# Kernel tuning notes

Hardware: AMD Instinct MI355X
Metric: run time of the kernel (lower is better)

The kernel has to match this reference:

```python
import jax, jax.numpy as jnp
import numpy as np
from jax import lax

HEADS = 8
DIM_HEAD = 64
INNER = HEADS * DIM_HEAD  # 512
DIM = 256
TOP_K = 512  # top_k=-1 -> Lk // heads = 4096 // 8
LN_EPS = 1e-5


def chan_ln(x, g, b):
    # LayerNorm over channel dim (axis=1) of [b,c,D,H,W]
    mu = jnp.mean(x, axis=1, keepdims=True)
    var = jnp.mean((x - mu) ** 2, axis=1, keepdims=True)
    xn = (x - mu) * lax.rsqrt(var + LN_EPS)
    return xn * g[None, :, None, None, None] + b[None, :, None, None, None]


def l1_cdist(K, Q):
    # K: [B,N,D], Q: [B,M,D] -> [B,N,M]; scan over feature dim to avoid a [B,N,M,D] intermediate
    Kt = jnp.moveaxis(K, -1, 0)  # [D,B,N]
    Qt = jnp.moveaxis(Q, -1, 0)  # [D,B,M]
    acc0 = jnp.zeros((K.shape[0], K.shape[1], Q.shape[1]), K.dtype)
    def step(acc, kq):
        kd, qd = kq
        return acc + jnp.abs(kd[:, :, None] - qd[:, None, :]), None
    acc, _ = lax.scan(step, acc0, (Kt, Qt))
    return acc


def l2norm_ax(t, axis):
    n = jnp.sqrt(jnp.sum(t * t, axis=axis, keepdims=True))
    return t / jnp.maximum(n, 1e-12)


def setup_inputs() -> dict:
    key = jax.random.key(0)
    ks = jax.random.split(key, 12)
    b, Dq, Hq, Wq = 2, 16, 32, 32
    Dc, Hc, Wc = 16, 16, 16
    Lk = Dc * Hc * Wc  # 4096
    return {
        "query_source": jax.random.normal(ks[0], (b, DIM, Dq, Hq, Wq), jnp.float32),
        "context": jax.random.normal(ks[1], (b, DIM, Dc, Hc, Wc), jnp.float32),
        "rand_idx": jax.random.randint(ks[2], (b * HEADS, TOP_K), 0, 4096),
        "g_ctx": jnp.ones((DIM,), jnp.float32),
        "b_ctx": jnp.zeros((DIM,), jnp.float32),
        "g_qs": jnp.ones((DIM,), jnp.float32),
        "b_qs": jnp.zeros((DIM,), jnp.float32),
        "w_kv": jax.random.normal(ks[3], (2 * INNER, DIM), jnp.float32) * 0.02,
        "w_q": jax.random.normal(ks[4], (INNER, DIM), jnp.float32) * 0.02,
        "w_out": jax.random.normal(ks[5], (DIM, INNER), jnp.float32) * 0.02,
        "g_out": jnp.ones((DIM,), jnp.float32),
        "b_out": jnp.zeros((DIM,), jnp.float32),
        "gamma": jnp.full((1,), 0.5, jnp.float32),
    }


def reference(query_source, context, rand_idx, g_ctx, b_ctx, g_qs, b_qs,
              w_kv, w_q, w_out, g_out, b_out, gamma):
    b, c, Dq, Hq, Wq = query_source.shape
    Lq = Dq * Hq * Wq
    Lk = context.shape[2] * context.shape[3] * context.shape[4]

    ctx = chan_ln(context, g_ctx, b_ctx)
    qsn = chan_ln(query_source, g_qs, b_qs)

    # 1x1x1 convs == channel matmuls
    kv = jnp.einsum('oc,bcdhw->bodhw', w_kv, ctx)
    k, v = jnp.split(kv, 2, axis=1)
    q = jnp.einsum('oc,bcdhw->bodhw', w_q, qsn)

    def fold(t):  # [b, inner, ...] -> [b, heads, dim_head, L]
        return t.reshape(t.shape[0], HEADS, DIM_HEAD, -1)
    q, k, v = fold(q), fold(k), fold(v)
    # l2norm over dim_head channels (torch dim=1 after (b h) fold)
    q = l2norm_ax(q, 2)
    k = l2norm_ax(k, 2)
    # -> [b, heads, L, dim_head]
    q = jnp.swapaxes(q, 2, 3)
    k = jnp.swapaxes(k, 2, 3)
    v = jnp.swapaxes(v, 2, 3)

    BH = b * HEADS
    qf = q.reshape(BH, Lq, DIM_HEAD)
    kf = k.reshape(BH, Lk, DIM_HEAD)
    vf = v.reshape(BH, Lk, DIM_HEAD)

    # random-query-anchored token pruning
    Q_small = jnp.take_along_axis(qf, rand_idx[:, :, None], axis=1)  # [BH, TOP_K, dh]
    dist = l1_cdist(kf, Q_small)                                     # [BH, Lk, TOP_K]
    min_d = jnp.min(dist, axis=2)                                    # [BH, Lk]
    _, idx = lax.top_k(-min_d, TOP_K)                                # smallest distances
    ks_sel = jnp.take_along_axis(kf, idx[:, :, None], axis=1)        # [BH, TOP_K, dh]
    vs_sel = jnp.take_along_axis(vf, idx[:, :, None], axis=1)

    ks4 = ks_sel.reshape(b, HEADS, TOP_K, DIM_HEAD)
    vs4 = vs_sel.reshape(b, HEADS, TOP_K, DIM_HEAD)

    # SDPA with scale=1.0, no dropout (eval)
    scores = jnp.einsum('bhqd,bhkd->bhqk', q, ks4)
    attn = jax.nn.softmax(scores, axis=-1)
    out = jnp.einsum('bhqk,bhkd->bhqd', attn, vs4)  # [b,H,Lq,dh]

    out = out.reshape(b, HEADS, Dq, Hq, Wq, DIM_HEAD)
    out = jnp.transpose(out, (0, 1, 5, 2, 3, 4)).reshape(b, INNER, Dq, Hq, Wq)
    out = jnp.einsum('oc,bcdhw->bodhw', w_out, out)
    out = chan_ln(out, g_out, b_out)
    return gamma[0] * out + query_source
```

## Files before the change

### kernel.cpp

```cpp
#include <hip/hip_runtime.h>
#include <hip/hip_bf16.h>
#include <math.h>

#define DIMC  256
#define HEADS 8
#define DH    64
#define INNER 512
#define TOPK  512
#define LQ    16384
#define LKE   4096
#define NB    2
#define NBH   16

typedef __attribute__((ext_vector_type(8))) short bf16x8;
typedef __attribute__((ext_vector_type(4))) float f32x4;
typedef __attribute__((ext_vector_type(16))) unsigned u32x16;

__device__ __forceinline__ unsigned short f2bf(float f) {
    unsigned u = __float_as_uint(f);
    u += 0x7FFFu + ((u >> 16) & 1u);
    return (unsigned short)(u >> 16);
}
__device__ __forceinline__ float bf2f(unsigned short b) {
    return __uint_as_float(((unsigned)b) << 16);
}
__device__ __forceinline__ f32x4 mfma16(bf16x8 a, bf16x8 b, f32x4 c) {
    return __builtin_amdgcn_mfma_f32_16x16x32_bf16(a, b, c, 0, 0, 0);
}
__device__ __forceinline__ unsigned f2q16(float v) {
    return (unsigned)((int)rintf(v * 32000.0f) + 32768) & 0xFFFFu;
}

__global__ void stats_all_kernel(const float* __restrict__ ctx, const float* __restrict__ qs,
                                 float* __restrict__ mu_c, float* __restrict__ rs_c,
                                 float* __restrict__ mu_q, float* __restrict__ rs_q) {
    int idx = blockIdx.x * 256 + threadIdx.x;
    const float* x; float* mu; float* rs; int L; int li;
    if (idx < NB * LKE) { x = ctx; mu = mu_c; rs = rs_c; L = LKE; li = idx; }
    else { li = idx - NB * LKE; if (li >= NB * LQ) return; x = qs; mu = mu_q; rs = rs_q; L = LQ; }
    int b = li / L, l = li - b * L;
    const float* p = x + (size_t)b * DIMC * L + l;
    float s = 0.f, sq = 0.f;
    for (int c = 0; c < DIMC; c++) {
        float v = p[(size_t)c * L];
        s += v; sq += v * v;
    }
    float m = s * (1.0f / DIMC);
    float var = fmaxf(sq * (1.0f / DIMC) - m * m, 0.f);
    mu[li] = m;
    rs[li] = rsqrtf(var + 1e-5f);
}

template<bool WRITELO>
__global__ __launch_bounds__(256) void ln_transpose_kernel(
    const float* __restrict__ x, const float* __restrict__ mu, const float* __restrict__ rs,
    const float* __restrict__ g, const float* __restrict__ beta, int L,
    unsigned short* __restrict__ xhi, unsigned short* __restrict__ xlo) {
    int lt = blockIdx.x, ct = blockIdx.y, b = blockIdx.z;
    int l0 = lt * 64, c0 = ct * 64;
    int t = threadIdx.x;
    __shared__ float T[64][65];
#pragma unroll
    for (int r = 0; r < 16; r++) {
        int f = r * 256 + t;
        int l = f & 63, c = f >> 6;
        int loc = b * L + l0 + l;
        float v = x[((size_t)b * DIMC + c0 + c) * L + l0 + l];
        T[c][l] = (v - mu[loc]) * rs[loc] * g[c0 + c] + beta[c0 + c];
    }
    __syncthreads();
#pragma unroll
    for (int r = 0; r < 16; r++) {
        int f = r * 256 + t;
        int c = f & 63, l = f >> 6;
        float v = T[c][l];
        unsigned short hi = f2bf(v);
        size_t di = ((size_t)b * L + l0 + l) * DIMC + c0 + c;
        xhi[di] = hi;
        if (WRITELO) xlo[di] = f2bf(v - bf2f(hi));
    }
}

template<int MODE>
__global__ __launch_bounds__(256) void gemm_mfma_kernel(
    const float* __restrict__ wmat,
    const unsigned short* __restrict__ xhi, const unsigned short* __restrict__ xlo,
    void* __restrict__ dst0, void* __restrict__ dst1, void* __restrict__ dst2) {
    constexpr int K = (MODE == 2) ? 512 : 256;
    constexpr int N = (MODE == 0) ? LKE : LQ;
    constexpr bool MAYSPLIT = (MODE == 0);
    int n0 = blockIdx.x * 128;
    int by = blockIdx.y;
    int bb = blockIdx.z;
    int t = threadIdx.x, w = t >> 6, lane = t & 63;
    int wm = w >> 1, wn = w & 1;
    int lanelo = lane & 15, lanehi = lane >> 4;

    __shared__ __align__(16) char Wh[16384];
    __shared__ __align__(16) char Xh[16384];
    __shared__ __align__(16) char Wl[MAYSPLIT ? 16384 : 16];
    __shared__ __align__(16) char Xl[MAYSPLIT ? 16384 : 16];

    bool split = MAYSPLIT && (by < 4);

    const float* wsrc = wmat + (size_t)by * 128 * K;
    const unsigned short* xsh = xhi + ((size_t)bb * N + n0) * K;
    const unsigned short* xsl = xlo + ((size_t)bb * N + n0) * K;

    f32x4 acc[4][4];
#pragma unroll
    for (int mi = 0; mi < 4; mi++)
#pragma unroll
        for (int ni = 0; ni < 4; ni++) acc[mi][ni] = (f32x4){0.f, 0.f, 0.f, 0.f};

    for (int k0 = 0; k0 < K; k0 += 64) {
        if (k0) __syncthreads();
#pragma unroll
        for (int gg = 0; gg < 4; gg++) {
            int e = gg * 2048 + t * 8;
            int row = e >> 6, kc = e & 63;
            const float* wp = wsrc + (size_t)row * K + k0 + kc;
            bf16x8 hi, lo;
#pragma unroll
            for (int i = 0; i < 8; i++) {
                float v = wp[i];
                unsigned short h = f2bf(v);
                hi[i] = (short)h;
                if (MAYSPLIT) lo[i] = (short)f2bf(v - bf2f(h));
            }
            int off = (row * 128 + kc * 2) ^ ((row & 7) << 4);
            *(bf16x8*)(Wh + off) = hi;
            *(bf16x8*)(Xh + off) = *(const bf16x8*)(xsh + (size_t)row * K + k0 + kc);
            if (split) {
                *(bf16x8*)(Wl + off) = lo;
                *(bf16x8*)(Xl + off) = *(const bf16x8*)(xsl + (size_t)row * K + k0 + kc);
            }
        }
        __syncthreads();
#pragma unroll
        for (int kk = 0; kk < 2; kk++) {
            bf16x8 ah[4], bh_[4];
#pragma unroll
            for (int mi = 0; mi < 4; mi++) {
                int row = wm * 64 + mi * 16 + lanelo;
                int off = (row * 128 + kk * 64 + lanehi * 16) ^ ((row & 7) << 4);
                ah[mi] = *(const bf16x8*)(Wh + off);
            }
#pragma unroll
            for (int ni = 0; ni < 4; ni++) {
                int row = wn * 64 + ni * 16 + lanelo;
                int off = (row * 128 + kk * 64 + lanehi * 16) ^ ((row & 7) << 4);
                bh_[ni] = *(const bf16x8*)(Xh + off);
            }
#pragma unroll
            for (int mi = 0; mi < 4; mi++)
#pragma unroll
                for (int ni = 0; ni < 4; ni++)
                    acc[mi][ni] = mfma16(ah[mi], bh_[ni], acc[mi][ni]);
            if (split) {
                bf16x8 al[4], bl_[4];
#pragma unroll
                for (int mi = 0; mi < 4; mi++) {
                    int row = wm * 64 + mi * 16 + lanelo;
                    int off = (row * 128 + kk * 64 + lanehi * 16) ^ ((row & 7) << 4);
                    al[mi] = *(const bf16x8*)(Wl + off);
                }
#pragma unroll
                for (int ni = 0; ni < 4; ni++) {
                    int row = wn * 64 + ni * 16 + lanelo;
                    int off = (row * 128 + kk * 64 + lanehi * 16) ^ ((row & 7) << 4);
                    bl_[ni] = *(const bf16x8*)(Xl + off);
                }
#pragma unroll
                for (int mi = 0; mi < 4; mi++)
#pragma unroll
                    for (int ni = 0; ni < 4; ni++) {
                        acc[mi][ni] = mfma16(ah[mi], bl_[ni], acc[mi][ni]);
                        acc[mi][ni] = mfma16(al[mi], bh_[ni], acc[mi][ni]);
                    }
            }
        }
    }

    bool donorm = (MODE == 1) || (MODE == 0 && by < 4);
    float inv[4];
    if (donorm) {
#pragma unroll
        for (int ni = 0; ni < 4; ni++) {
            float s = 0.f;
#pragma unroll
            for (int mi = 0; mi < 4; mi++)
#pragma unroll
                for (int rg = 0; rg < 4; rg++) s += acc[mi][ni][rg] * acc[mi][ni][rg];
            s += __shfl_xor(s, 16);
            s += __shfl_xor(s, 32);
            inv[ni] = 1.0f / fmaxf(sqrtf(s), 1e-12f);
        }
    }
#pragma unroll
    for (int mi = 0; mi < 4; mi++) {
        int rowg = by * 128 + wm * 64 + mi * 16 + lanehi * 4;
#pragma unroll
        for (int ni = 0; ni < 4; ni++) {
            int l = n0 + wn * 64 + ni * 16 + lanelo;
            if (MODE == 0) {
                bool isk = rowg < 512;
                float sc = isk ? inv[ni] : 1.0f;
                int h = (rowg >> 6) & 7, d0 = rowg & 63;
                float4 v = make_float4(acc[mi][ni][0] * sc, acc[mi][ni][1] * sc,
                                       acc[mi][ni][2] * sc, acc[mi][ni][3] * sc);
                float* dp = isk ? (float*)dst0 : (float*)dst1;
                size_t base = ((size_t)(bb * HEADS + h) * LKE + l) * 64 + d0;
                *(float4*)&dp[base] = v;
                if (isk) {
                    uint2 pk;
                    pk.x = f2q16(v.x) | (f2q16(v.y) << 16);
                    pk.y = f2q16(v.z) | (f2q16(v.w) << 16);
                    *(uint2*)&((unsigned*)dst2)[(((size_t)(bb * HEADS + h) * LKE + l) * 64 + d0) / 2] = pk;
                }
            } else if (MODE == 1) {
                int h = rowg >> 6, d0 = rowg & 63;
                ushort4 u;
                u.x = f2bf(acc[mi][ni][0] * inv[ni]);
                u.y = f2bf(acc[mi][ni][1] * inv[ni]);
                u.z = f2bf(acc[mi][ni][2] * inv[ni]);
                u.w = f2bf(acc[mi][ni][3] * inv[ni]);
                unsigned short* qp = (unsigned short*)dst0;
                *(ushort4*)&qp[((size_t)(bb * HEADS + h) * LQ + l) * 64 + d0] = u;
            } else {
                float4 v = make_float4(acc[mi][ni][0], acc[mi][ni][1],
                                       acc[mi][ni][2], acc[mi][ni][3]);
                float* pp = (float*)dst0;
                *(float4*)&pp[((size_t)bb * LQ + l) * 256 + rowg] = v;
            }
        }
    }
}

__global__ __launch_bounds__(256) void qsample_kernel(
    const float* __restrict__ x, const float* __restrict__ mu, const float* __restrict__ rs,
    const float* __restrict__ g, const float* __restrict__ beta,
    const float* __restrict__ w, const int* __restrict__ ridx,
    unsigned* __restrict__ Qint) {
    int lt = blockIdx.x, bh = blockIdx.y;
    int b = bh >> 3, h = bh & 7;
    int t = threadIdx.x, tx = t & 15, ty = t >> 4;
    __shared__ float Ws[64][33];
    __shared__ float Xs[32][65];
    __shared__ float Cs[64][65];
    __shared__ float nf[64];
    __shared__ int lidx[64];
    if (t < 64) lidx[t] = ridx[bh * TOPK + lt * 64 + t];
    __syncthreads();
    float acc[4][4];
#pragma unroll
    for (int a = 0; a < 4; a++)
#pragma unroll
        for (int c2 = 0; c2 < 4; c2++) acc[a][c2] = 0.f;
    for (int kc = 0; kc < DIMC; kc += 32) {
#pragma unroll
        for (int r = 0; r < 8; r++) {
            int f = r * 256 + t;
            int oi = f >> 5, kj = f & 31;
            Ws[oi][kj] = w[(size_t)(h * 64 + oi) * DIMC + kc + kj];
        }
#pragma unroll
        for (int r = 0; r < 8; r++) {
            int f = r * 256 + t;
            int kj = f >> 6, lj = f & 63;
            int l = lidx[lj];
            int loc = b * LQ + l;
            float v = x[(size_t)b * DIMC * LQ + (size_t)(kc + kj) * LQ + l];
            Xs[kj][lj] = (v - mu[loc]) * rs[loc] * g[kc + kj] + beta[kc + kj];
        }
        __syncthreads();
#pragma unroll
        for (int kj = 0; kj < 32; kj++) {
            float wr[4], xr[4];
#pragma unroll
            for (int a = 0; a < 4; a++) wr[a] = Ws[ty * 4 + a][kj];
#pragma unroll
            for (int c2 = 0; c2 < 4; c2++) xr[c2] = Xs[kj][tx * 4 + c2];
#pragma unroll
            for (int a = 0; a < 4; a++)
#pragma unroll
                for (int c2 = 0; c2 < 4; c2++) acc[a][c2] += wr[a] * xr[c2];
        }
        __syncthreads();
    }
#pragma unroll
    for (int a = 0; a < 4; a++)
#pragma unroll
        for (int c2 = 0; c2 < 4; c2++) Cs[ty * 4 + a][tx * 4 + c2] = acc[a][c2];
    __syncthreads();
    if (t < 64) {
        float sq = 0.f;
        for (int o = 0; o < 64; o++) { float v = Cs[o][t]; sq += v * v; }
        nf[t] = 1.0f / fmaxf(sqrtf(sq), 1e-12f);
    }
    __syncthreads();
#pragma unroll
    for (int r = 0; r < 8; r++) {
        int f = r * 256 + t;
        int dp = f & 31, lj = f >> 5;
        float v0 = Cs[dp * 2][lj] * nf[lj];
        float v1 = Cs[dp * 2 + 1][lj] * nf[lj];
        Qint[((size_t)bh * TOPK + (size_t)lt * 64 + lj) * 32 + dp] =
            f2q16(v0) | (f2q16(v1) << 16);
    }
}

__global__ __launch_bounds__(256) __attribute__((amdgpu_waves_per_eu(4, 4)))
void cdist_sad_kernel(
    const unsigned* __restrict__ kint,
    const unsigned* __restrict__ Qint,
    unsigned* __restrict__ min_d4) {
    int bh = blockIdx.y;
    int key = blockIdx.x * 256 + threadIdx.x;
    int qz = blockIdx.z;
    const unsigned* kp = kint + ((size_t)bh * LKE + key) * 32;
    unsigned k[32];
#pragma unroll
    for (int d8 = 0; d8 < 8; d8++) {
        uint4 v = *(const uint4*)(kp + d8 * 4);
        k[d8 * 4 + 0] = v.x; k[d8 * 4 + 1] = v.y;
        k[d8 * 4 + 2] = v.z; k[d8 * 4 + 3] = v.w;
    }
#pragma unroll
    for (int d = 0; d < 32; d++) asm volatile("" : "+v"(k[d]));

    unsigned long long qaddr = (unsigned long long)(const void*)
        (Qint + ((size_t)bh * TOPK + (size_t)qz * (TOPK / 4)) * 32);
    u32x16 qa0, qa1, qb0, qb1;
    asm volatile(
        "s_load_dwordx16 %0, %2, 0x00\n\t"
        "s_load_dwordx16 %1, %2, 0x40"
        : "=s"(qa0), "=s"(qa1) : "s"(qaddr));
    unsigned best = 0xFFFFFFFFu;

#define S1(ACC, KK, QQ) asm("v_sad_u16 %0, %1, %2, %0" : "+v"(ACC) : "v"(KK), "s"(QQ));
#define S16(QV, KB) \
    S1(a0, k[KB + 0], QV[0])  S1(a1, k[KB + 1], QV[1]) \
    S1(a2, k[KB + 2], QV[2])  S1(a3, k[KB + 3], QV[3]) \
    S1(a0, k[KB + 4], QV[4])  S1(a1, k[KB + 5], QV[5]) \
    S1(a2, k[KB + 6], QV[6])  S1(a3, k[KB + 7], QV[7]) \
    S1(a0, k[KB + 8], QV[8])  S1(a1, k[KB + 9], QV[9]) \
    S1(a2, k[KB + 10], QV[10]) S1(a3, k[KB + 11], QV[11]) \
    S1(a0, k[KB + 12], QV[12]) S1(a1, k[KB + 13], QV[13]) \
    S1(a2, k[KB + 14], QV[14]) S1(a3, k[KB + 15], QV[15])

    for (int qi = 0; qi < TOPK / 4; qi += 2) {
        asm volatile(
            "s_load_dwordx16 %0, %2, 0x80\n\t"
            "s_load_dwordx16 %1, %2, 0xc0"
            : "=s"(qb0), "=s"(qb1) : "s"(qaddr));
        asm volatile("s_waitcnt lgkmcnt(2)" : "+s"(qa0), "+s"(qa1));
        {
            unsigned a0 = 0, a1 = 0, a2 = 0, a3 = 0;
            S16(qa0, 0) S16(qa1, 16)
            best = min(best, (a0 + a1) + (a2 + a3));
        }
        qaddr += 256;
        asm volatile(
            "s_load_dwordx16 %0, %2, 0x00\n\t"
            "s_load_dwordx16 %1, %2, 0x40"
            : "=s"(qa0), "=s"(qa1) : "s"(qaddr));
        asm volatile("s_waitcnt lgkmcnt(2)" : "+s"(qb0), "+s"(qb1));
        {
            unsigned a0 = 0, a1 = 0, a2 = 0, a3 = 0;
            S16(qb0, 0) S16(qb1, 16)
            best = min(best, (a0 + a1) + (a2 + a3));
        }
    }
#undef S16
#undef S1
    min_d4[((size_t)qz * NBH + bh) * LKE + key] = best;
}

__global__ void select_topk_kernel(const unsigned* __restrict__ min_d4, int* __restrict__ isel) {
    int bh = blockIdx.x;
    int t = threadIdx.x;
    __shared__ unsigned su[LKE];
    __shared__ int hist[256];
    __shared__ int scan[256];
    __shared__ int sb[2];
    for (int i = t; i < LKE; i += 256) {
        unsigned a = min(min_d4[(size_t)bh * LKE + i],
                         min_d4[(size_t)(NBH + bh) * LKE + i]);
        unsigned b = min(min_d4[(size_t)(2 * NBH + bh) * LKE + i],
                         min_d4[(size_t)(3 * NBH + bh) * LKE + i]);
        su[i] = min(a, b);
    }
    unsigned prefix = 0, mask = 0;
    int need = TOPK;
    for (int shift = 24; shift >= 0; shift -= 8) {
        hist[t] = 0;
        __syncthreads();
        for (int i = t; i < LKE; i += 256) {
            unsigned u = su[i];
            if ((u & mask) == prefix) atomicAdd(&hist[(u >> shift) & 255], 1);
        }
        __syncthreads();
        scan[t] = hist[t];
        __syncthreads();
#pragma unroll
        for (int d = 1; d < 256; d <<= 1) {
            int v = (t >= d) ? scan[t - d] : 0;
            __syncthreads();
            scan[t] += v;
            __syncthreads();
        }
        int excl = (t == 0) ? 0 : scan[t - 1];
        if (scan[t] >= need && excl < need) {
            sb[0] = t;
            sb[1] = need - excl;
        }
        __syncthreads();
        prefix |= ((unsigned)sb[0]) << shift;
        mask |= (255u << shift);
        need = sb[1];
        __syncthreads();
    }
    if (t < 64) {
        int pos = 0, eqseen = 0;
        unsigned long long lanem1 = (t == 0) ? 0ull : ((1ull << t) - 1ull);
        for (int i0 = 0; i0 < LKE; i0 += 64) {
            unsigned u = su[i0 + t];
            bool lt = (u < prefix);
            bool eq = (u == prefix);
            unsigned long long be = __ballot(eq);
            int eqbefore = __popcll(be & lanem1);
            bool take = lt || (eq && (eqseen + eqbefore) < need);
            unsigned long long bt = __ballot(take);
            if (take) isel[bh * TOPK + pos + __popcll(bt & lanem1)] = i0 + t;
            pos += __popcll(bt);
            eqseen += __popcll(be);
        }
    }
}

__global__ __launch_bounds__(256) void gather_kv_kernel(
    const float* __restrict__ kf, const float* __restrict__ vf,
    const int* __restrict__ isel,
    unsigned short* __restrict__ kselh, unsigned short* __restrict__ vTh) {
    int bh = blockIdx.y, kc = blockIdx.x * 64;
    int t = threadIdx.x;
    __shared__ float T[64][65];
    __shared__ int rows[64];
    if (t < 64) rows[t] = isel[bh * TOPK + kc + t];
    __syncthreads();
#pragma unroll
    for (int r = 0; r < 16; r++) {
        int f = r * 256 + t;
        int key = f >> 6, d = f & 63;
        kselh[((size_t)bh * TOPK + kc + key) * 64 + d] =
            f2bf(kf[((size_t)bh * LKE + rows[key]) * 64 + d]);
    }
#pragma unroll
    for (int r = 0; r < 4; r++) {
        int c = r * 256 + t;
        int row = c >> 4, c4 = c & 15;
        float4 v = *(const float4*)(vf + ((size_t)bh * LKE + rows[row]) * 64 + c4 * 4);
        T[row][c4 * 4 + 0] = v.x; T[row][c4 * 4 + 1] = v.y;
        T[row][c4 * 4 + 2] = v.z; T[row][c4 * 4 + 3] = v.w;
    }
    __syncthreads();
#pragma unroll
    for (int r = 0; r < 16; r++) {
        int f = r * 256 + t;
        int d = f >> 6, key = f & 63;
        vTh[(size_t)bh * 64 * TOPK + (size_t)d * TOPK + kc + key] = f2bf(T[key][d]);
    }
}

__global__ __launch_bounds__(256) void attn_mfma_kernel(
    const unsigned short* __restrict__ qh,
    const unsigned short* __restrict__ kselh,
    const unsigned short* __restrict__ vTh,
    unsigned short* __restrict__ afT) {
    int bh = blockIdx.y, rt = blockIdx.x;
    int bq = bh >> 3, h = bh & 7;
    int t = threadIdx.x, w = t >> 6, lane = t & 63;
    __shared__ unsigned short Ks[2][64 * 64];
    __shared__ unsigned short Vts[2][64 * 64];
    __shared__ unsigned short Ps[4][2][16 * 64];

    const unsigned short* qb = qh + ((size_t)bh * LQ + (size_t)rt * 128) * 64;
    const unsigned short* kb = kselh + (size_t)bh * TOPK * 64;
    const unsigned short* vb = vTh + (size_t)bh * 64 * TOPK;

    int lanelo = lane & 15, lanehi = lane >> 4;

    int row0s = t >> 3, c80 = t & 7;
    int row1s = 32 + (t >> 3), c81 = t & 7;
    int offs0 = (row0s * 128 + c80 * 16) ^ ((row0s & 7) << 4);
    int offs1 = (row1s * 128 + c81 * 16) ^ ((row1s & 7) << 4);

    bf16x8 qfrag[2][2];
#pragma unroll
    for (int s = 0; s < 2; s++)
#pragma unroll
        for (int kk = 0; kk < 2; kk++) {
            int row = s * 64 + w * 16 + lanelo;
            qfrag[s][kk] = *(const bf16x8*)(qb + (size_t)row * 64 + kk * 32 + lanehi * 8);
        }

    {
        *(bf16x8*)((char*)Ks[0] + offs0) = *(const bf16x8*)(kb + row0s * 64 + c80 * 8);
        *(bf16x8*)((char*)Ks[0] + offs1) = *(const bf16x8*)(kb + row1s * 64 + c81 * 8);
        *(bf16x8*)((char*)Vts[0] + offs0) = *(const bf16x8*)(vb + row0s * TOPK + c80 * 8);
        *(bf16x8*)((char*)Vts[0] + offs1) = *(const bf16x8*)(vb + row1s * TOPK + c81 * 8);
    }
    __syncthreads();

    f32x4 o[2][4];
#pragma unroll
    for (int s = 0; s < 2; s++)
#pragma unroll
        for (int m = 0; m < 4; m++) o[s][m] = (f32x4){0.f, 0.f, 0.f, 0.f};
    float part[2][4] = {{0.f, 0.f, 0.f, 0.f}, {0.f, 0.f, 0.f, 0.f}};
    int cur = 0;

    for (int ch = 0; ch < 8; ch++) {
        bf16x8 knx0, knx1, vnx0, vnx1;
        if (ch < 7) {
            int kc0 = (ch + 1) * 64;
            knx0 = *(const bf16x8*)(kb + (kc0 + row0s) * 64 + c80 * 8);
            knx1 = *(const bf16x8*)(kb + (kc0 + row1s) * 64 + c81 * 8);
            vnx0 = *(const bf16x8*)(vb + row0s * TOPK + kc0 + c80 * 8);
            vnx1 = *(const bf16x8*)(vb + row1s * TOPK + kc0 + c81 * 8);
        }
        bf16x8 kfr[4][2];
#pragma unroll
        for (int n = 0; n < 4; n++)
#pragma unroll
            for (int kk = 0; kk < 2; kk++) {
                int row = n * 16 + lanelo;
                kfr[n][kk] = *(const bf16x8*)((char*)Ks[cur] +
                    ((row * 128 + kk * 64 + lanehi * 16) ^ ((row & 7) << 4)));
            }
#pragma unroll
        for (int s = 0; s < 2; s++) {
            f32x4 sv[4];
#pragma unroll
            for (int n = 0; n < 4; n++) {
                sv[n] = (f32x4){0.f, 0.f, 0.f, 0.f};
#pragma unroll
                for (int kk = 0; kk < 2; kk++)
                    sv[n] = mfma16(qfrag[s][kk], kfr[n][kk], sv[n]);
            }
            unsigned short* pw = Ps[w][s];
#pragma unroll
            for (int n = 0; n < 4; n++) {
#pragma unroll
                for (int rg = 0; rg < 4; rg++) {
                    float p = __expf(sv[n][rg]);
                    unsigned short ph = (unsigned short)(__float_as_uint(p) >> 16);
                    part[s][rg] += bf2f(ph);
                    int row = lanehi * 4 + rg, col = n * 16 + lanelo;
                    *(unsigned short*)((char*)pw +
                        ((row * 128 + col * 2) ^ ((row & 7) << 4))) = ph;
                }
            }
        }
        bf16x8 vfr[4][2];
#pragma unroll
        for (int m = 0; m < 4; m++)
#pragma unroll
            for (int kk = 0; kk < 2; kk++) {
                int row = m * 16 + lanelo;
                vfr[m][kk] = *(const bf16x8*)((char*)Vts[cur] +
                    ((row * 128 + kk * 64 + lanehi * 16) ^ ((row & 7) << 4)));
            }
#pragma unroll
        for (int s = 0; s < 2; s++) {
            bf16x8 pfrag[2];
#pragma unroll
            for (int kk = 0; kk < 2; kk++) {
                int row = lanelo;
                pfrag[kk] = *(const bf16x8*)((char*)Ps[w][s] +
                    ((row * 128 + kk * 64 + lanehi * 16) ^ ((row & 7) << 4)));
            }
#pragma unroll
            for (int m = 0; m < 4; m++)
#pragma unroll
                for (int kk = 0; kk < 2; kk++)
                    o[s][m] = mfma16(pfrag[kk], vfr[m][kk], o[s][m]);
        }
        if (ch < 7) {
            *(bf16x8*)((char*)Ks[cur ^ 1] + offs0) = knx0;
            *(bf16x8*)((char*)Ks[cur ^ 1] + offs1) = knx1;
            *(bf16x8*)((char*)Vts[cur ^ 1] + offs0) = vnx0;
            *(bf16x8*)((char*)Vts[cur ^ 1] + offs1) = vnx1;
        }
        __syncthreads();
        cur ^= 1;
    }
#pragma unroll
    for (int s = 0; s < 2; s++) {
#pragma unroll
        for (int rg = 0; rg < 4; rg++) {
            float v = part[s][rg];
            v += __shfl_xor(v, 1); v += __shfl_xor(v, 2);
            v += __shfl_xor(v, 4); v += __shfl_xor(v, 8);
            float invs = 1.0f / v;
            int l = rt * 128 + s * 64 + w * 16 + lanehi * 4 + rg;
            size_t base = ((size_t)bq * LQ + l) * 512 + h * 64 + lanelo;
#pragma unroll
            for (int m = 0; m < 4; m++)
                afT[base + m * 16] = f2bf(o[s][m][rg] * invs);
        }
    }
}

__global__ void stats_loc_kernel(const float* __restrict__ pre, float* __restrict__ mu,
                                 float* __restrict__ rs) {
    int t = threadIdx.x;
    int grp = t >> 4, ln = t & 15;
    int loc = blockIdx.x * 16 + grp;
    const float4* p = (const float4*)(pre + (size_t)loc * 256);
    float s = 0.f, sq = 0.f;
#pragma unroll
    for (int i = 0; i < 4; i++) {
        float4 v = p[ln + i * 16];
        s += v.x + v.y + v.z + v.w;
        sq += v.x * v.x + v.y * v.y + v.z * v.z + v.w * v.w;
    }
#pragma unroll
    for (int d = 1; d < 16; d <<= 1) {
        s += __shfl_xor(s, d);
        sq += __shfl_xor(sq, d);
    }
    if (ln == 0) {
        float m = s * (1.0f / 256.0f);
        float var = fmaxf(sq * (1.0f / 256.0f) - m * m, 0.f);
        mu[loc] = m;
        rs[loc] = rsqrtf(var + 1e-5f);
    }
}

__global__ __launch_bounds__(256) void final_kernel(
    const float* __restrict__ pre, const float* __restrict__ mu,
    const float* __restrict__ rs, const float* __restrict__ g,
    const float* __restrict__ beta, const float* __restrict__ gamma,
    const float* __restrict__ qs_in, float* __restrict__ out) {
    int lt = blockIdx.x, ot = blockIdx.y, b = blockIdx.z;
    int l0 = lt * 64, o0 = ot * 64;
    int t = threadIdx.x;
    __shared__ float T[64][65];
    float gm = gamma[0];
#pragma unroll
    for (int r = 0; r < 16; r++) {
        int f = r * 256 + t;
        int o = f & 63, l = f >> 6;
        int loc = b * LQ + l0 + l;
        float v = pre[(size_t)loc * 256 + o0 + o];
        T[o][l] = ((v - mu[loc]) * rs[loc] * g[o0 + o] + beta[o0 + o]) * gm;
    }
    __syncthreads();
#pragma unroll
    for (int r = 0; r < 16; r++) {
        int f = r * 256 + t;
        int l = f & 63, o = f >> 6;
        size_t oi = ((size_t)(b * DIMC + o0 + o)) * LQ + l0 + l;
        out[oi] = T[o][l] + qs_in[oi];
    }
}

extern "C" void kernel_launch(void* const* d_in, const int* in_sizes, int n_in,
                              void* d_out, int out_size, void* d_ws, size_t ws_size,
                              hipStream_t stream) {
    const float* qs_in = (const float*)d_in[0];
    const float* ctx   = (const float*)d_in[1];
    const int*   ridx  = (const int*)d_in[2];
    const float* g_ctx = (const float*)d_in[3];
    const float* b_ctx = (const float*)d_in[4];
    const float* g_qs  = (const float*)d_in[5];
    const float* b_qs  = (const float*)d_in[6];
    const float* w_kv  = (const float*)d_in[7];
    const float* w_q   = (const float*)d_in[8];
    const float* w_out = (const float*)d_in[9];
    const float* g_out = (const float*)d_in[10];
    const float* b_out = (const float*)d_in[11];
    const float* gamma = (const float*)d_in[12];
    float* out = (float*)d_out;

    char* ws = (char*)d_ws;
    size_t off = 0;
    auto alloc = [&](size_t bytes) { char* p = ws + off; off += (bytes + 255) & ~(size_t)255; return p; };

    float*          kf    = (float*)alloc((size_t)NBH * LKE * 64 * 4);
    float*          vf    = (float*)alloc((size_t)NBH * LKE * 64 * 4);
    unsigned*       kint  = (unsigned*)alloc((size_t)NBH * LKE * 32 * 4);
    unsigned short* qh    = (unsigned short*)alloc((size_t)NBH * LQ * 64 * 2);
    char*           uni   = alloc((size_t)NB * LQ * INNER * 2);
    unsigned short* ctxT_hi = (unsigned short*)(uni);
    unsigned short* ctxT_lo = (unsigned short*)(uni + (size_t)NB * LKE * DIMC * 2);
    unsigned short* qsT_hi  = (unsigned short*)(uni + (size_t)2 * NB * LKE * DIMC * 2);
    unsigned short* afT     = (unsigned short*)(uni);

    unsigned*       Qint  = (unsigned*)alloc((size_t)NBH * TOPK * 32 * 4);
    unsigned short* kselh = (unsigned short*)alloc((size_t)NBH * TOPK * 64 * 2);
    unsigned short* vTh   = (unsigned short*)alloc((size_t)NBH * 64 * TOPK * 2);
    float*          pre   = (float*)alloc((size_t)NB * LQ * DIMC * 4);
    unsigned*       min_d4= (unsigned*)alloc((size_t)4 * NBH * LKE * 4);
    float*          mu_c  = (float*)alloc(NB * LKE * 4);
    float*          rs_c  = (float*)alloc(NB * LKE * 4);
    float*          mu_q  = (float*)alloc(NB * LQ * 4);
    float*          rs_q  = (float*)alloc(NB * LQ * 4);
    float*          mu_o  = (float*)alloc(NB * LQ * 4);
    float*          rs_o  = (float*)alloc(NB * LQ * 4);
    int*            isel  = (int*)alloc(NBH * TOPK * 4);

    stats_all_kernel<<<(NB * (LKE + LQ)) / 256, 256, 0, stream>>>(
        ctx, qs_in, mu_c, rs_c, mu_q, rs_q);
    ln_transpose_kernel<true><<<dim3(LKE / 64, DIMC / 64, NB), 256, 0, stream>>>(
        ctx, mu_c, rs_c, g_ctx, b_ctx, LKE, ctxT_hi, ctxT_lo);
    ln_transpose_kernel<false><<<dim3(LQ / 64, DIMC / 64, NB), 256, 0, stream>>>(
        qs_in, mu_q, rs_q, g_qs, b_qs, LQ, qsT_hi, nullptr);
    gemm_mfma_kernel<0><<<dim3(LKE / 128, 8, NB), 256, 0, stream>>>(
        w_kv, ctxT_hi, ctxT_lo, kf, vf, kint);
    gemm_mfma_kernel<1><<<dim3(LQ / 128, 4, NB), 256, 0, stream>>>(
        w_q, qsT_hi, qsT_hi, qh, nullptr, nullptr);
    qsample_kernel<<<dim3(TOPK / 64, NBH), 256, 0, stream>>>(
        qs_in, mu_q, rs_q, g_qs, b_qs, w_q, ridx, Qint);
    cdist_sad_kernel<<<dim3(LKE / 256, NBH, 4), 256, 0, stream>>>(kint, Qint, min_d4);
    select_topk_kernel<<<NBH, 256, 0, stream>>>(min_d4, isel);
    gather_kv_kernel<<<dim3(TOPK / 64, NBH), 256, 0, stream>>>(kf, vf, isel, kselh, vTh);
    attn_mfma_kernel<<<dim3(LQ / 128, NBH), 256, 0, stream>>>(qh, kselh, vTh, afT);
    gemm_mfma_kernel<2><<<dim3(LQ / 128, 2, NB), 256, 0, stream>>>(
        w_out, afT, afT, pre, nullptr, nullptr);
    stats_loc_kernel<<<(NB * LQ) / 16, 256, 0, stream>>>(pre, mu_o, rs_o);
    final_kernel<<<dim3(LQ / 64, DIMC / 64, NB), 256, 0, stream>>>(
        pre, mu_o, rs_o, g_out, b_out, gamma, qs_in, out);
}
```

Before: 310.8 us.

## Fuse output projection GEMM with channel LayerNorm and residual epilogue

Replaces the separate output GEMM, per-location stats kernel and final LN/residual kernel with one kernel. Each block owns 64 query locations across all 256 output channels, so the LayerNorm statistics can be reduced in registers and LDS and written straight to the NCHW output. This removes the fp32 'pre' intermediate round trip and two launches. In exchange, the block reconverts the full fp32 w_out to bf16 on every k-step, grid size shrinks, and output stores along l are 16-wide per lane group rather than fully coalesced.

```diff
diff --git a/kernel.cpp b/kernel.cpp
--- a/kernel.cpp
+++ b/kernel.cpp
@@ -86,7 +86,7 @@
     const float* __restrict__ wmat,
     const unsigned short* __restrict__ xhi, const unsigned short* __restrict__ xlo,
     void* __restrict__ dst0, void* __restrict__ dst1, void* __restrict__ dst2) {
-    constexpr int K = (MODE == 2) ? 512 : 256;
+    constexpr int K = 256;
     constexpr int N = (MODE == 0) ? LKE : LQ;
     constexpr bool MAYSPLIT = (MODE == 0);
     int n0 = blockIdx.x * 128;
@@ -218,7 +218,7 @@
                     pk.y = f2q16(v.z) | (f2q16(v.w) << 16);
                     *(uint2*)&((unsigned*)dst2)[(((size_t)(bb * HEADS + h) * LKE + l) * 64 + d0) / 2] = pk;
                 }
-            } else if (MODE == 1) {
+            } else {
                 int h = rowg >> 6, d0 = rowg & 63;
                 ushort4 u;
                 u.x = f2bf(acc[mi][ni][0] * inv[ni]);
@@ -227,11 +227,124 @@
                 u.w = f2bf(acc[mi][ni][3] * inv[ni]);
                 unsigned short* qp = (unsigned short*)dst0;
                 *(ushort4*)&qp[((size_t)(bb * HEADS + h) * LQ + l) * 64 + d0] = u;
-            } else {
-                float4 v = make_float4(acc[mi][ni][0], acc[mi][ni][1],
-                                       acc[mi][ni][2], acc[mi][ni][3]);
-                float* pp = (float*)dst0;
-                *(float4*)&pp[((size_t)bb * LQ + l) * 256 + rowg] = v;
+            }
+        }
+    }
+}
+
+__global__ __launch_bounds__(256) void gemm_out_fused_kernel(
+    const float* __restrict__ wmat,
+    const unsigned short* __restrict__ afT,
+    const float* __restrict__ g, const float* __restrict__ beta,
+    const float* __restrict__ gamma, const float* __restrict__ qs_in,
+    float* __restrict__ out) {
+    int l0 = blockIdx.x * 64;
+    int b  = blockIdx.y;
+    int t = threadIdx.x, w = t >> 6, lane = t & 63;
+    int lanelo = lane & 15, lanehi = lane >> 4;
+
+    __shared__ __align__(16) char Wh[32768];
+    __shared__ __align__(16) char Xh[8192];
+    __shared__ float sLds[4][64];
+    __shared__ float sqLds[4][64];
+    __shared__ float gs[256], bs[256];
+
+    gs[t] = g[t];
+    bs[t] = beta[t];
+
+    const unsigned short* xs = afT + ((size_t)b * LQ + l0) * 512;
+
+    f32x4 acc[4][4];
+#pragma unroll
+    for (int mi = 0; mi < 4; mi++)
+#pragma unroll
+        for (int ni = 0; ni < 4; ni++) acc[mi][ni] = (f32x4){0.f, 0.f, 0.f, 0.f};
+
+    int row0s = t >> 3, c80 = t & 7;
+    int row1s = 32 + (t >> 3);
+    int offs0 = (row0s * 128 + c80 * 16) ^ ((row0s & 7) << 4);
+    int offs1 = (row1s * 128 + c80 * 16) ^ ((row1s & 7) << 4);
+
+    for (int k0 = 0; k0 < 512; k0 += 64) {
+        if (k0) __syncthreads();
+#pragma unroll
+        for (int gg = 0; gg < 8; gg++) {
+            int row = gg * 32 + (t >> 3);
+            int kc = (t & 7) * 8;
+            const float* wp = wmat + (size_t)row * 512 + k0 + kc;
+            bf16x8 hi;
+#pragma unroll
+            for (int i = 0; i < 8; i++) hi[i] = (short)f2bf(wp[i]);
+            int off = (row * 128 + kc * 2) ^ ((row & 7) << 4);
+            *(bf16x8*)(Wh + off) = hi;
+        }
+        *(bf16x8*)(Xh + offs0) = *(const bf16x8*)(xs + (size_t)row0s * 512 + k0 + c80 * 8);
+        *(bf16x8*)(Xh + offs1) = *(const bf16x8*)(xs + (size_t)row1s * 512 + k0 + c80 * 8);
+        __syncthreads();
+#pragma unroll
+        for (int kk = 0; kk < 2; kk++) {
+            bf16x8 ah[4], bh_[4];
+#pragma unroll
+            for (int mi = 0; mi < 4; mi++) {
+                int row = w * 64 + mi * 16 + lanelo;
+                int off = (row * 128 + kk * 64 + lanehi * 16) ^ ((row & 7) << 4);
+                ah[mi] = *(const bf16x8*)(Wh + off);
+            }
+#pragma unroll
+            for (int ni = 0; ni < 4; ni++) {
+                int row = ni * 16 + lanelo;
+                int off = (row * 128 + kk * 64 + lanehi * 16) ^ ((row & 7) << 4);
+                bh_[ni] = *(const bf16x8*)(Xh + off);
+            }
+#pragma unroll
+            for (int mi = 0; mi < 4; mi++)
+#pragma unroll
+                for (int ni = 0; ni < 4; ni++)
+                    acc[mi][ni] = mfma16(ah[mi], bh_[ni], acc[mi][ni]);
+        }
+    }
+
+#pragma unroll
+    for (int ni = 0; ni < 4; ni++) {
+        float s = 0.f, sq = 0.f;
+#pragma unroll
+        for (int mi = 0; mi < 4; mi++)
+#pragma unroll
+            for (int rg = 0; rg < 4; rg++) {
+                float v = acc[mi][ni][rg];
+                s += v; sq += v * v;
+            }
+        s += __shfl_xor(s, 16);  s += __shfl_xor(s, 32);
+        sq += __shfl_xor(sq, 16); sq += __shfl_xor(sq, 32);
+        if (lanehi == 0) {
+            sLds[w][ni * 16 + lanelo] = s;
+            sqLds[w][ni * 16 + lanelo] = sq;
+        }
+    }
+    __syncthreads();
+    float mu_[4], rs_[4];
+#pragma unroll
+    for (int ni = 0; ni < 4; ni++) {
+        int l = ni * 16 + lanelo;
+        float s  = (sLds[0][l] + sLds[1][l]) + (sLds[2][l] + sLds[3][l]);
+        float sq = (sqLds[0][l] + sqLds[1][l]) + (sqLds[2][l] + sqLds[3][l]);
+        float m = s * (1.0f / 256.0f);
+        float var = fmaxf(sq * (1.0f / 256.0f) - m * m, 0.f);
+        mu_[ni] = m;
+        rs_[ni] = rsqrtf(var + 1e-5f);
+    }
+    float gm = gamma[0];
+#pragma unroll
+    for (int mi = 0; mi < 4; mi++) {
+#pragma unroll
+        for (int ni = 0; ni < 4; ni++) {
+            int l = ni * 16 + lanelo;
+#pragma unroll
+            for (int rg = 0; rg < 4; rg++) {
+                int ch = w * 64 + mi * 16 + lanehi * 4 + rg;
+                float xn = (acc[mi][ni][rg] - mu_[ni]) * rs_[ni] * gs[ch] + bs[ch];
+                size_t oi = ((size_t)(b * DIMC + ch)) * LQ + l0 + l;
+                out[oi] = gm * xn + qs_in[oi];
             }
         }
     }
@@ -610,60 +723,6 @@
             for (int m = 0; m < 4; m++)
                 afT[base + m * 16] = f2bf(o[s][m][rg] * invs);
         }
-    }
-}
-
-__global__ void stats_loc_kernel(const float* __restrict__ pre, float* __restrict__ mu,
-                                 float* __restrict__ rs) {
-    int t = threadIdx.x;
-    int grp = t >> 4, ln = t & 15;
-    int loc = blockIdx.x * 16 + grp;
-    const float4* p = (const float4*)(pre + (size_t)loc * 256);
-    float s = 0.f, sq = 0.f;
-#pragma unroll
-    for (int i = 0; i < 4; i++) {
-        float4 v = p[ln + i * 16];
-        s += v.x + v.y + v.z + v.w;
-        sq += v.x * v.x + v.y * v.y + v.z * v.z + v.w * v.w;
-    }
-#pragma unroll
-    for (int d = 1; d < 16; d <<= 1) {
-        s += __shfl_xor(s, d);
-        sq += __shfl_xor(sq, d);
-    }
-    if (ln == 0) {
-        float m = s * (1.0f / 256.0f);
-        float var = fmaxf(sq * (1.0f / 256.0f) - m * m, 0.f);
-        mu[loc] = m;
-        rs[loc] = rsqrtf(var + 1e-5f);
-    }
-}
-
-__global__ __launch_bounds__(256) void final_kernel(
-    const float* __restrict__ pre, const float* __restrict__ mu,
-    const float* __restrict__ rs, const float* __restrict__ g,
-    const float* __restrict__ beta, const float* __restrict__ gamma,
-    const float* __restrict__ qs_in, float* __restrict__ out) {
-    int lt = blockIdx.x, ot = blockIdx.y, b = blockIdx.z;
-    int l0 = lt * 64, o0 = ot * 64;
-    int t = threadIdx.x;
-    __shared__ float T[64][65];
-    float gm = gamma[0];
-#pragma unroll
-    for (int r = 0; r < 16; r++) {
-        int f = r * 256 + t;
-        int o = f & 63, l = f >> 6;
-        int loc = b * LQ + l0 + l;
-        float v = pre[(size_t)loc * 256 + o0 + o];
-        T[o][l] = ((v - mu[loc]) * rs[loc] * g[o0 + o] + beta[o0 + o]) * gm;
-    }
-    __syncthreads();
-#pragma unroll
-    for (int r = 0; r < 16; r++) {
-        int f = r * 256 + t;
-        int l = f & 63, o = f >> 6;
-        size_t oi = ((size_t)(b * DIMC + o0 + o)) * LQ + l0 + l;
-        out[oi] = T[o][l] + qs_in[oi];
     }
 }
 
@@ -702,14 +761,11 @@
     unsigned*       Qint  = (unsigned*)alloc((size_t)NBH * TOPK * 32 * 4);
     unsigned short* kselh = (unsigned short*)alloc((size_t)NBH * TOPK * 64 * 2);
     unsigned short* vTh   = (unsigned short*)alloc((size_t)NBH * 64 * TOPK * 2);
-    float*          pre   = (float*)alloc((size_t)NB * LQ * DIMC * 4);
     unsigned*       min_d4= (unsigned*)alloc((size_t)4 * NBH * LKE * 4);
     float*          mu_c  = (float*)alloc(NB * LKE * 4);
     float*          rs_c  = (float*)alloc(NB * LKE * 4);
     float*          mu_q  = (float*)alloc(NB * LQ * 4);
     float*          rs_q  = (float*)alloc(NB * LQ * 4);
-    float*          mu_o  = (float*)alloc(NB * LQ * 4);
-    float*          rs_o  = (float*)alloc(NB * LQ * 4);
     int*            isel  = (int*)alloc(NBH * TOPK * 4);
 
     stats_all_kernel<<<(NB * (LKE + LQ)) / 256, 256, 0, stream>>>(
@@ -728,9 +784,6 @@
     select_topk_kernel<<<NBH, 256, 0, stream>>>(min_d4, isel);
     gather_kv_kernel<<<dim3(TOPK / 64, NBH), 256, 0, stream>>>(kf, vf, isel, kselh, vTh);
     attn_mfma_kernel<<<dim3(LQ / 128, NBH), 256, 0, stream>>>(qh, kselh, vTh, afT);
-    gemm_mfma_kernel<2><<<dim3(LQ / 128, 2, NB), 256, 0, stream>>>(
-        w_out, afT, afT, pre, nullptr, nullptr);
-    stats_loc_kernel<<<(NB * LQ) / 16, 256, 0, stream>>>(pre, mu_o, rs_o);
-    final_kernel<<<dim3(LQ / 64, DIMC / 64, NB), 256, 0, stream>>>(
-        pre, mu_o, rs_o, g_out, b_out, gamma, qs_in, out);
-}
+    gemm_out_fused_kernel<<<dim3(LQ / 64, NB), 256, 0, stream>>>(
+        w_out, afT, g_out, b_out, gamma, qs_in, out);
+}
```

Result: faster. 299.0 us, median of 3 (-3.8%).
